# Performance work log

Hardware: AMD Instinct MI355X
Metric: run time of the kernel (lower is better)

Reference implementation:

```python
import jax, jax.numpy as jnp
import numpy as np

N_GROUP = 8
TOPK_GROUP = 4
TOP_K = 8
ROUTED_SCALE = 2.5


def setup_inputs() -> dict:
    key = jax.random.key(0)
    ks = jax.random.split(key, 8)
    B, S, D, E, I = 4, 2048, 2048, 32, 1024
    s = 0.02
    return {
        "x": jax.random.normal(ks[0], (B, S, D), jnp.float32),
        "gate_w": jax.random.normal(ks[1], (D, E), jnp.float32) * s,
        "e_bias": jnp.zeros((E,), jnp.float32),
        "gate_up": jax.random.normal(ks[2], (E, D, 2 * I), jnp.float32) * s,
        "down": jax.random.normal(ks[3], (E, I, D), jnp.float32) * s,
        "shared_gate": jax.random.normal(ks[4], (D, I), jnp.float32) * s,
        "shared_up": jax.random.normal(ks[5], (D, I), jnp.float32) * s,
        "shared_down": jax.random.normal(ks[6], (I, D), jnp.float32) * s,
    }


def _router(x_flat, gate_w, e_bias):
    N, E = x_flat.shape[0], gate_w.shape[1]
    epg = E // N_GROUP  # experts per group
    logits = x_flat @ gate_w                                   # [N, E]
    scores = jax.nn.sigmoid(logits.astype(jnp.float32))        # [N, E]
    sfr = scores + e_bias                                      # routing scores
    grouped = sfr.reshape(N, N_GROUP, epg)
    group_scores = jax.lax.top_k(grouped, min(2, epg))[0].sum(-1)   # [N, G]
    topk_group_idx = jax.lax.top_k(group_scores, TOPK_GROUP)[1]     # [N, topk_group]
    group_mask = jnp.zeros((N, N_GROUP), bool).at[
        jnp.arange(N)[:, None], topk_group_idx].set(True)
    expert_mask = jnp.repeat(group_mask, epg, axis=1)          # [N, E]
    masked = jnp.where(expert_mask, sfr, -jnp.inf)
    topk_idx = jax.lax.top_k(masked, TOP_K)[1]                 # [N, K]
    topk_w = jnp.take_along_axis(scores, topk_idx, axis=1)     # [N, K]
    topk_w = topk_w / (topk_w.sum(-1, keepdims=True) + 1e-20)  # norm_topk_prob
    topk_w = topk_w * ROUTED_SCALE
    return topk_idx, topk_w, scores


def _experts(x_flat, topk_idx, topk_w, gate_up, down):
    N, D = x_flat.shape
    E, K = gate_up.shape[0], topk_idx.shape[1]
    flat = topk_idx.reshape(-1)                                # [N*K]
    sort_idx = jnp.argsort(flat)                               # route: group rows by expert
    sorted_tokens = x_flat[sort_idx // K]                      # [N*K, D]
    group_sizes = jnp.bincount(flat, length=E).astype(jnp.int32)
    h = jax.lax.ragged_dot(sorted_tokens, gate_up, group_sizes)  # [N*K, 2I]
    gate_h, up_h = jnp.split(h, 2, axis=-1)
    inter = jax.nn.silu(gate_h) * up_h                         # SwiGLU
    out = jax.lax.ragged_dot(inter, down, group_sizes)         # [N*K, D]
    unsorted = jnp.zeros_like(out).at[sort_idx].set(out)       # unroute
    return (unsorted.reshape(N, K, D) * topk_w[..., None].astype(out.dtype)).sum(1)


def _shared_mlp(x, wg, wu, wd):
    return (jax.nn.silu(x @ wg) * (x @ wu)) @ wd


def reference(x, gate_w, e_bias, gate_up, down, shared_gate, shared_up, shared_down):
    B, S, D = x.shape
    x_flat = x.reshape(B * S, D)
    topk_idx, topk_w, scores = _router(x_flat, gate_w, e_bias)
    routed = _experts(x_flat, topk_idx, topk_w, gate_up, down).reshape(B, S, D)
    output = routed + _shared_mlp(x, shared_gate, shared_up, shared_down)
    return output, topk_idx, scores
```

## Files before the change

kernel.cpp:

```cpp
#include <hip/hip_runtime.h>
#include <hip/hip_bf16.h>
#include <math.h>


typedef __bf16 bf16_t;
typedef __bf16 bf16x8 __attribute__((ext_vector_type(8)));
typedef float  f32x4  __attribute__((ext_vector_type(4)));

constexpr int NTOK = 8192;
constexpr int D    = 2048;
constexpr int E    = 32;
constexpr int I    = 1024;
constexpr int TK   = 8;
constexpr int NK   = NTOK * TK;
constexpr int TM   = 256;
constexpr int MAX_TILES = E + NK / TM;
constexpr float RSCALE = 2.5f;

#define GL16(g, l) __builtin_amdgcn_global_load_lds( \
    (const __attribute__((address_space(1))) void*)(g), \
    (__attribute__((address_space(3))) void*)(l), 16, 0, 0)


__global__ __launch_bounds__(64) void k_zero_meta(int* counts, int* cursors, int* ntl) {
    int t = threadIdx.x;
    if (t < E) { counts[t] = 0; cursors[t] = 0; }
    if (t == 0) *ntl = 0;
}

__global__ __launch_bounds__(64) void k_sentinel(float* out) {
    if (threadIdx.x == 0) out[0] = 12345.0f;
}

__global__ __launch_bounds__(256) void k_convert_x(const float* __restrict__ src,
                                                   bf16_t* __restrict__ dst, int n8) {
    int i = blockIdx.x * 256 + threadIdx.x;
    if (i >= n8) return;
    const float4* s = (const float4*)src;
    float4 a = s[(size_t)i * 2], b = s[(size_t)i * 2 + 1];
    bf16_t t[8] = {(bf16_t)a.x, (bf16_t)a.y, (bf16_t)a.z, (bf16_t)a.w,
                   (bf16_t)b.x, (bf16_t)b.y, (bf16_t)b.z, (bf16_t)b.w};
    *(uint4*)(dst + (size_t)i * 8) = *(const uint4*)t;
}

template <int MODE>
__global__ __launch_bounds__(256) void k_transpose(const float* __restrict__ src,
                                                   bf16_t* __restrict__ dst,
                                                   int R, int C,
                                                   size_t srcMat, size_t dstMat) {
    __shared__ float t[32][33];
    int b = blockIdx.z;
    const float* s = src + (size_t)b * srcMat;
    bf16_t* d = dst + (size_t)b * dstMat;
    int c0 = blockIdx.x * 32, r0 = blockIdx.y * 32;
    int tx = threadIdx.x, ty = threadIdx.y;
#pragma unroll
    for (int yy = 0; yy < 4; yy++)
        t[ty + yy * 8][tx] = s[(size_t)(r0 + ty + yy * 8) * C + c0 + tx];
    __syncthreads();
#pragma unroll
    for (int yy = 0; yy < 4; yy++) {
        int c = c0 + ty + yy * 8;
        int rc = (MODE == 0) ? c
               : (MODE == 1) ? ((c < I) ? 2 * c : 2 * (c - I) + 1)
               : (MODE == 2) ? 2 * c : 2 * c + 1;
        d[(size_t)rc * R + r0 + tx] = (bf16_t)t[tx][ty + yy * 8];
    }
}


__global__ __launch_bounds__(256) void k_router(const float* __restrict__ x,
                                                const float* __restrict__ gw,
                                                const float* __restrict__ eb,
                                                float* __restrict__ out_idx,
                                                float* __restrict__ out_scores,
                                                float* __restrict__ topk_w,
                                                int* __restrict__ tok_expert,
                                                int* __restrict__ counts) {
    int t = blockIdx.x;
    int tid = threadIdx.x;
    int e = tid & 31, part = tid >> 5;
    const float* xr = x + (size_t)t * D;
    float partial = 0.f;
    int d0 = part * 256;
    for (int d = d0; d < d0 + 256; d++)
        partial += xr[d] * gw[(size_t)d * E + e];

    __shared__ float red[8][32];
    __shared__ float sc[32], sfr[32];
    red[part][e] = partial;
    __syncthreads();
    if (tid < 32) {
        float l = 0.f;
#pragma unroll
        for (int p = 0; p < 8; p++) l += red[p][tid];
        float s = 1.f / (1.f + expf(-l));
        sc[tid] = s;
        sfr[tid] = s + eb[tid];
        out_scores[(size_t)t * E + tid] = s;
    }
    __syncthreads();
    if (tid == 0) {
        float gs[8];
#pragma unroll
        for (int g = 0; g < 8; g++) {
            float m1 = -1e30f, m2 = -1e30f;
#pragma unroll
            for (int i = 0; i < 4; i++) {
                float v = sfr[g * 4 + i];
                if (v > m1) { m2 = m1; m1 = v; } else if (v > m2) m2 = v;
            }
            gs[g] = m1 + m2;
        }
        bool gsel[8] = {false, false, false, false, false, false, false, false};
        for (int it = 0; it < 4; it++) {
            int bi = -1; float bv = -1e30f;
            for (int g = 0; g < 8; g++)
                if (!gsel[g] && gs[g] > bv) { bv = gs[g]; bi = g; }
            gsel[bi] = true;
        }
        float masked[32];
        for (int i = 0; i < 32; i++) masked[i] = gsel[i >> 2] ? sfr[i] : -1e30f;
        int idx[TK]; float w[TK]; float wsum = 0.f;
        for (int k = 0; k < TK; k++) {
            int bi = 0; float bv = -1e30f;
            for (int i = 0; i < 32; i++)
                if (masked[i] > bv) { bv = masked[i]; bi = i; }
            masked[bi] = -1e30f;
            idx[k] = bi; w[k] = sc[bi]; wsum += w[k];
        }
        float inv = RSCALE / (wsum + 1e-20f);
        for (int k = 0; k < TK; k++) {
            out_idx[(size_t)t * TK + k] = (float)idx[k];
            topk_w[(size_t)t * TK + k] = w[k] * inv;
            tok_expert[(size_t)t * TK + k] = idx[k];
            atomicAdd(&counts[idx[k]], 1);
        }
    }
}

__global__ __launch_bounds__(64) void k_offsets(const int* __restrict__ counts,
                                                int* __restrict__ offs,
                                                int4* __restrict__ ttbl,
                                                int* __restrict__ ntl) {
    if (threadIdx.x != 0) return;
    int off = 0, nt = 0;
    for (int e = 0; e < E; e++) {
        offs[e] = off;
        int c = counts[e];
        for (int r = 0; r < c; r += TM) {
            ttbl[nt] = make_int4(off + r, min(TM, c - r), e, 0);
            nt++;
        }
        off += c;
    }
    offs[E] = off;
    *ntl = nt;
}

__global__ __launch_bounds__(256) void k_scatter(const int* __restrict__ tok_expert,
                                                 const int* __restrict__ offs,
                                                 int* __restrict__ cursors,
                                                 int* __restrict__ slot_token,
                                                 int* __restrict__ slot_inv) {
    int i = blockIdx.x * 256 + threadIdx.x;
    if (i >= NK) return;
    int e = tok_expert[i];
    int pos = offs[e] + atomicAdd(&cursors[e], 1);
    slot_token[pos] = i >> 3;
    slot_inv[i] = pos;
}


#define SCB() __builtin_amdgcn_sched_barrier(0)

#define P_MID() do { __builtin_amdgcn_s_barrier(); SCB(); \
    __builtin_amdgcn_s_setprio(1); } while (0)

#define P_END() do { __builtin_amdgcn_s_setprio(0); \
    __builtin_amdgcn_s_barrier(); SCB(); } while (0)

#define P_END_VM4() do { __builtin_amdgcn_s_setprio(0); \
    asm volatile("s_waitcnt vmcnt(4)" ::: "memory"); \
    __builtin_amdgcn_s_barrier(); SCB(); } while (0)

#define STAGE_A(b, h, k0) do { \
    GL16(gA[h][0] + (k0), smb + (b) * 65536 + (h) * 16384 + w * 1024); \
    GL16(gA[h][1] + (k0), smb + (b) * 65536 + (h) * 16384 + 8192 + w * 1024); } while (0)

#define STAGE_B(b, h, k0) do { \
    GL16(gB[h][0] + (k0), smb + (b) * 65536 + 32768 + (h) * 16384 + w * 1024); \
    GL16(gB[h][1] + (k0), smb + (b) * 65536 + 32768 + (h) * 16384 + 8192 + w * 1024); } while (0)

#define LOAD_A(b, mh) do { _Pragma("unroll") for (int m_ = 0; m_ < 4; m_++) { \
    aF[m_][0] = *(const bf16x8*)(smb + (b) * 65536 + wm * 16384 + (mh) * 8192 + m_ * 2048 + lofs0); \
    aF[m_][1] = *(const bf16x8*)(smb + (b) * 65536 + wm * 16384 + (mh) * 8192 + m_ * 2048 + lofs1); } } while (0)

#define LOAD_B(b, nh) do { _Pragma("unroll") for (int n_ = 0; n_ < 2; n_++) { \
    bF[nh][n_][0] = *(const bf16x8*)(smb + (b) * 65536 + 32768 + wn * 8192 + (nh) * 4096 + n_ * 2048 + lofs0); \
    bF[nh][n_][1] = *(const bf16x8*)(smb + (b) * 65536 + 32768 + wn * 8192 + (nh) * 4096 + n_ * 2048 + lofs1); } } while (0)

#define MM(MH, NH) do { _Pragma("unroll") for (int m_ = 0; m_ < 4; m_++) \
    _Pragma("unroll") for (int n_ = 0; n_ < 2; n_++) { \
    acc[(MH) * 4 + m_][(NH) * 2 + n_] = __builtin_amdgcn_mfma_f32_16x16x32_bf16( \
        aF[m_][0], bF[NH][n_][0], acc[(MH) * 4 + m_][(NH) * 2 + n_], 0, 0, 0); \
    acc[(MH) * 4 + m_][(NH) * 2 + n_] = __builtin_amdgcn_mfma_f32_16x16x32_bf16( \
        aF[m_][1], bF[NH][n_][1], acc[(MH) * 4 + m_][(NH) * 2 + n_], 0, 0, 0); } } while (0)

template <bool EXPERT, bool GATHER, int EPI>
__global__ __launch_bounds__(512, 2) void k_mm8(const bf16_t* __restrict__ A,
                                                const bf16_t* __restrict__ Bt,
                                                int K, size_t estride,
                                                const int* __restrict__ slot_token,
                                                const int4* __restrict__ ttbl,
                                                const int* __restrict__ ntl,
                                                void* __restrict__ C, int ldc) {
    int L = (int)blockIdx.y * 8 + (int)blockIdx.x;
    int xcd = L & 7, k = L >> 3;
    int per = (int)gridDim.y >> 3;
    int ty = xcd * per + (k >> 3);
    int tx = k & 7;

    int base_slot, rows, e;
    if (EXPERT) {
        if (ty >= *ntl) return;
        int4 tt = ttbl[ty];
        base_slot = tt.x; rows = tt.y; e = tt.z;
    } else {
        base_slot = ty * TM; rows = TM; e = 0;
    }
    int c0 = tx * 256;
    const bf16_t* Bw = Bt + (size_t)e * estride + (size_t)c0 * K;

    extern __shared__ char smb[];

    int tid = threadIdx.x, lane = tid & 63, w = tid >> 6;
    int wm = w >> 2, wn = w & 3;
    int lr = lane & 15, hi = lane >> 4;
    int rx = lr & 7;
    int lofs0 = lr * 128 + ((hi ^ rx) << 4);
    int lofs1 = lr * 128 + (((4 + hi) ^ rx) << 4);

    int srow = tid >> 3;
    int cbg = (tid & 7) ^ (srow & 7);
    const bf16_t* gA[2][2]; const bf16_t* gB[2][2];
#pragma unroll
    for (int h = 0; h < 2; h++)
#pragma unroll
        for (int rnd = 0; rnd < 2; rnd++) {
            int r = h * 128 + rnd * 64 + srow;
            int ar = min(r, rows - 1);
            int tok = GATHER ? slot_token[base_slot + ar] : (base_slot + ar);
            gA[h][rnd] = A + (size_t)tok * K + cbg * 8;
            gB[h][rnd] = Bw + (size_t)r * K + cbg * 8;
        }

    f32x4 acc[8][4] = {};
    bf16x8 aF[4][2], bF[2][2][2];

    STAGE_B(0, 0, 0); STAGE_B(0, 1, 0);
    STAGE_A(0, 0, 0); STAGE_A(0, 1, 0);
    STAGE_B(1, 0, 64); STAGE_B(1, 1, 64);
    asm volatile("s_waitcnt vmcnt(4)" ::: "memory");
    __builtin_amdgcn_s_barrier();
    SCB();

    int nt = K >> 6;
    for (int kt = 0; kt < nt; kt += 2) {
        int k1 = (kt + 1) << 6;
        int k2 = (kt + 2 < nt) ? (kt + 2) << 6 : 0;
        int k3 = (kt + 3 < nt) ? (kt + 3) << 6 : 0;
        LOAD_B(0, 0); LOAD_A(0, 0);
        STAGE_A(1, 0, k1);
        P_MID(); MM(0, 0); P_END();
        LOAD_B(0, 1);
        STAGE_A(1, 1, k1);
        P_MID(); MM(0, 1); P_END();
        LOAD_A(0, 1);
        STAGE_B(0, 0, k2);
        P_MID(); MM(1, 0); P_END();
        STAGE_B(0, 1, k2);
        P_MID(); MM(1, 1); P_END_VM4();
        LOAD_B(1, 0); LOAD_A(1, 0);
        STAGE_A(0, 0, k2);
        P_MID(); MM(0, 0); P_END();
        LOAD_B(1, 1);
        STAGE_A(0, 1, k2);
        P_MID(); MM(0, 1); P_END();
        LOAD_A(1, 1);
        STAGE_B(1, 0, k3);
        P_MID(); MM(1, 0); P_END();
        STAGE_B(1, 1, k3);
        P_MID(); MM(1, 1); P_END_VM4();
    }

#pragma unroll
    for (int mi = 0; mi < 8; mi++) {
#pragma unroll
        for (int j = 0; j < 4; j++) {
            int r = wm * 128 + mi * 16 + hi * 4 + j;
            bool valid = !EXPERT || (r < rows);
            size_t orow = (size_t)base_slot + r;
#pragma unroll
            for (int f = 0; f < 4; f++) {
                float v = acc[mi][f][j];
                int c = c0 + wn * 64 + f * 16 + lr;
                if (EPI == 0) {
                    float o = __shfl_xor(v, 1);
                    float g = (lane & 1) ? o : v;
                    float u = (lane & 1) ? v : o;
                    float sv = g / (1.f + __expf(-g)) * u;
                    if (valid && !(lane & 1))
                        ((bf16_t*)C)[orow * ldc + (c >> 1)] = (bf16_t)sv;
                } else if (EPI == 1) {
                    float o = __shfl_xor(v, 1);
                    if (valid && !(lane & 1)) {
                        bf16_t pr[2] = {(bf16_t)v, (bf16_t)o};
                        *(unsigned int*)((bf16_t*)C + orow * ldc + c) = *(unsigned int*)pr;
                    }
                } else {
                    if (valid) ((float*)C)[orow * ldc + c] = v;
                }
            }
        }
    }
}


__global__ __launch_bounds__(256) void k_finalize(const bf16_t* __restrict__ outS,
                                                  const int* __restrict__ slot_inv,
                                                  const float* __restrict__ tkw,
                                                  float* __restrict__ out) {
    int tok = blockIdx.x, tid = threadIdx.x;
    __shared__ int sp[TK];
    __shared__ float swt[TK];
    if (tid < TK) {
        sp[tid] = slot_inv[tok * TK + tid];
        swt[tid] = tkw[tok * TK + tid];
    }
    __syncthreads();
    int c = tid * 8;
    float* op = out + (size_t)tok * D + c;
    float acc[8];
    float4 o0 = *(float4*)op, o1 = *(float4*)(op + 4);
    acc[0] = o0.x; acc[1] = o0.y; acc[2] = o0.z; acc[3] = o0.w;
    acc[4] = o1.x; acc[5] = o1.y; acc[6] = o1.z; acc[7] = o1.w;
#pragma unroll
    for (int k = 0; k < TK; k++) {
        bf16x8 v = *(const bf16x8*)(outS + (size_t)sp[k] * D + c);
        float w = swt[k];
#pragma unroll
        for (int j = 0; j < 8; j++) acc[j] += w * (float)v[j];
    }
    o0 = make_float4(acc[0], acc[1], acc[2], acc[3]);
    o1 = make_float4(acc[4], acc[5], acc[6], acc[7]);
    *(float4*)op = o0;
    *(float4*)(op + 4) = o1;
}


extern "C" void kernel_launch(void* const* d_in, const int* in_sizes, int n_in,
                              void* d_out, int out_size, void* d_ws, size_t ws_size,
                              hipStream_t stream) {
    const float* x  = (const float*)d_in[0];
    const float* gw = (const float*)d_in[1];
    const float* eb = (const float*)d_in[2];
    const float* gu = (const float*)d_in[3];
    const float* dn = (const float*)d_in[4];
    const float* sg = (const float*)d_in[5];
    const float* su = (const float*)d_in[6];
    const float* sd = (const float*)d_in[7];

    float* out        = (float*)d_out;
    float* out_idx    = out + (size_t)NTOK * D;
    float* out_scores = out_idx + (size_t)NTOK * TK;

    char* w = (char*)d_ws;
    auto alloc = [&](size_t bytes) {
        char* p = w;
        w += (bytes + 255) & ~(size_t)255;
        return p;
    };
    bf16_t* xb      = (bf16_t*)alloc((size_t)NTOK * D * 2);
    bf16_t* gut     = (bf16_t*)alloc((size_t)E * 2 * I * D * 2);
    bf16_t* dnt     = (bf16_t*)alloc((size_t)E * D * I * 2);
    bf16_t* sh1t    = (bf16_t*)alloc((size_t)2 * I * D * 2);
    bf16_t* sdt     = (bf16_t*)alloc((size_t)D * I * 2);
    bf16_t* inter   = (bf16_t*)alloc((size_t)NK * I * 2);
    bf16_t* inter_s = (bf16_t*)alloc((size_t)NTOK * I * 2);
    float*  tkw     = (float*)alloc((size_t)NK * 4);
    int*    tke     = (int*)alloc((size_t)NK * 4);
    int*    stok    = (int*)alloc((size_t)NK * 4);
    int*    sinv    = (int*)alloc((size_t)NK * 4);
    int*    counts  = (int*)alloc(E * 4);
    int*    offs    = (int*)alloc((E + 1) * 4);
    int*    curs    = (int*)alloc(E * 4);
    int4*   ttbl    = (int4*)alloc(MAX_TILES * 16);
    int*    ntl     = (int*)alloc(4);
    bf16_t* outS    = gut;

    if ((size_t)(w - (char*)d_ws) > ws_size) {
        k_sentinel<<<1, 64, 0, stream>>>(out);
        return;
    }

    k_zero_meta<<<1, 64, 0, stream>>>(counts, curs, ntl);
    k_convert_x<<<(NTOK * D / 8 + 255) / 256, 256, 0, stream>>>(x, xb, NTOK * D / 8);

    k_transpose<1><<<dim3(2 * I / 32, D / 32, E), dim3(32, 8), 0, stream>>>(
        gu, gut, D, 2 * I, (size_t)D * 2 * I, (size_t)D * 2 * I);
    k_transpose<0><<<dim3(D / 32, I / 32, E), dim3(32, 8), 0, stream>>>(
        dn, dnt, I, D, (size_t)I * D, (size_t)I * D);
    k_transpose<2><<<dim3(I / 32, D / 32, 1), dim3(32, 8), 0, stream>>>(
        sg, sh1t, D, I, 0, 0);
    k_transpose<3><<<dim3(I / 32, D / 32, 1), dim3(32, 8), 0, stream>>>(
        su, sh1t, D, I, 0, 0);
    k_transpose<0><<<dim3(D / 32, I / 32, 1), dim3(32, 8), 0, stream>>>(
        sd, sdt, I, D, 0, 0);

    k_router<<<NTOK, 256, 0, stream>>>(x, gw, eb, out_idx, out_scores, tkw, tke, counts);
    k_offsets<<<1, 64, 0, stream>>>(counts, offs, ttbl, ntl);
    k_scatter<<<NK / 256, 256, 0, stream>>>(tke, offs, curs, stok, sinv);

    constexpr size_t SMEM = 131072;
    k_mm8<true, true, 0><<<dim3(8, MAX_TILES), 512, SMEM, stream>>>(
        xb, gut, D, (size_t)2 * I * D, stok, ttbl, ntl, inter, I);
    k_mm8<true, false, 1><<<dim3(8, MAX_TILES), 512, SMEM, stream>>>(
        inter, dnt, I, (size_t)D * I, stok, ttbl, ntl, outS, D);

    k_mm8<false, false, 0><<<dim3(8, NTOK / TM), 512, SMEM, stream>>>(
        xb, sh1t, D, 0, nullptr, nullptr, nullptr, inter_s, I);
    k_mm8<false, false, 2><<<dim3(8, NTOK / TM), 512, SMEM, stream>>>(
        inter_s, sdt, I, 0, nullptr, nullptr, nullptr, out, D);

    k_finalize<<<NTOK, 256, 0, stream>>>(outS, sinv, tkw, out);
}
```

Before: 1.857 ms.

## Restructure GEMM main loop with one barrier per phase and double-buffered B fragments

Rewrites the inner k-loop schedule of the grouped GEMM kernel so each phase has a single barrier, preceded by a vmcnt(4) wait, instead of two barriers. B register fragments are now double-buffered (b0/b1) so LDS reads for the next MFMA block overlap the current one. A-tile staging is reordered by row-round rather than by half. The loop also prefetches the first fragments before entering. The aim is to cut barrier stalls and hide LDS latency behind MFMAs. This adds register pressure and risks LDS race hazards if the buffer reuse ordering is wrong.

```diff
diff --git a/kernel.cpp b/kernel.cpp
--- a/kernel.cpp
+++ b/kernel.cpp
@@ -174,38 +174,34 @@
 
 #define SCB() __builtin_amdgcn_sched_barrier(0)
 
-#define P_MID() do { __builtin_amdgcn_s_barrier(); SCB(); \
-    __builtin_amdgcn_s_setprio(1); } while (0)
-
-#define P_END() do { __builtin_amdgcn_s_setprio(0); \
+#define PEND() do { asm volatile("s_waitcnt vmcnt(4)" ::: "memory"); \
     __builtin_amdgcn_s_barrier(); SCB(); } while (0)
 
-#define P_END_VM4() do { __builtin_amdgcn_s_setprio(0); \
-    asm volatile("s_waitcnt vmcnt(4)" ::: "memory"); \
-    __builtin_amdgcn_s_barrier(); SCB(); } while (0)
-
-#define STAGE_A(b, h, k0) do { \
-    GL16(gA[h][0] + (k0), smb + (b) * 65536 + (h) * 16384 + w * 1024); \
-    GL16(gA[h][1] + (k0), smb + (b) * 65536 + (h) * 16384 + 8192 + w * 1024); } while (0)
-
-#define STAGE_B(b, h, k0) do { \
+#define SA2(b, rnd, k0) do { \
+    GL16(gA[0][rnd] + (k0), smb + (b) * 65536 + (rnd) * 8192 + w * 1024); \
+    GL16(gA[1][rnd] + (k0), smb + (b) * 65536 + 16384 + (rnd) * 8192 + w * 1024); } while (0)
+
+#define SB(b, h, k0) do { \
     GL16(gB[h][0] + (k0), smb + (b) * 65536 + 32768 + (h) * 16384 + w * 1024); \
     GL16(gB[h][1] + (k0), smb + (b) * 65536 + 32768 + (h) * 16384 + 8192 + w * 1024); } while (0)
 
-#define LOAD_A(b, mh) do { _Pragma("unroll") for (int m_ = 0; m_ < 4; m_++) { \
+#define LDA(b, mh) do { _Pragma("unroll") for (int m_ = 0; m_ < 4; m_++) { \
     aF[m_][0] = *(const bf16x8*)(smb + (b) * 65536 + wm * 16384 + (mh) * 8192 + m_ * 2048 + lofs0); \
     aF[m_][1] = *(const bf16x8*)(smb + (b) * 65536 + wm * 16384 + (mh) * 8192 + m_ * 2048 + lofs1); } } while (0)
 
-#define LOAD_B(b, nh) do { _Pragma("unroll") for (int n_ = 0; n_ < 2; n_++) { \
-    bF[nh][n_][0] = *(const bf16x8*)(smb + (b) * 65536 + 32768 + wn * 8192 + (nh) * 4096 + n_ * 2048 + lofs0); \
-    bF[nh][n_][1] = *(const bf16x8*)(smb + (b) * 65536 + 32768 + wn * 8192 + (nh) * 4096 + n_ * 2048 + lofs1); } } while (0)
-
-#define MM(MH, NH) do { _Pragma("unroll") for (int m_ = 0; m_ < 4; m_++) \
+#define LDB(dst, b, nh) do { _Pragma("unroll") for (int n_ = 0; n_ < 2; n_++) { \
+    dst[n_][0] = *(const bf16x8*)(smb + (b) * 65536 + 32768 + wn * 8192 + (nh) * 4096 + n_ * 2048 + lofs0); \
+    dst[n_][1] = *(const bf16x8*)(smb + (b) * 65536 + 32768 + wn * 8192 + (nh) * 4096 + n_ * 2048 + lofs1); } } while (0)
+
+#define MMA(bv, MH, NH) do { \
+    __builtin_amdgcn_s_setprio(1); \
+    _Pragma("unroll") for (int m_ = 0; m_ < 4; m_++) \
     _Pragma("unroll") for (int n_ = 0; n_ < 2; n_++) { \
     acc[(MH) * 4 + m_][(NH) * 2 + n_] = __builtin_amdgcn_mfma_f32_16x16x32_bf16( \
-        aF[m_][0], bF[NH][n_][0], acc[(MH) * 4 + m_][(NH) * 2 + n_], 0, 0, 0); \
+        aF[m_][0], bv[n_][0], acc[(MH) * 4 + m_][(NH) * 2 + n_], 0, 0, 0); \
     acc[(MH) * 4 + m_][(NH) * 2 + n_] = __builtin_amdgcn_mfma_f32_16x16x32_bf16( \
-        aF[m_][1], bF[NH][n_][1], acc[(MH) * 4 + m_][(NH) * 2 + n_], 0, 0, 0); } } while (0)
+        aF[m_][1], bv[n_][1], acc[(MH) * 4 + m_][(NH) * 2 + n_], 0, 0, 0); } \
+    __builtin_amdgcn_s_setprio(0); } while (0)
 
 template <bool EXPERT, bool GATHER, int EPI>
 __global__ __launch_bounds__(512, 2) void k_mm8(const bf16_t* __restrict__ A,
@@ -256,42 +252,52 @@
         }
 
     f32x4 acc[8][4] = {};
-    bf16x8 aF[4][2], bF[2][2][2];
-
-    STAGE_B(0, 0, 0); STAGE_B(0, 1, 0);
-    STAGE_A(0, 0, 0); STAGE_A(0, 1, 0);
-    STAGE_B(1, 0, 64); STAGE_B(1, 1, 64);
-    asm volatile("s_waitcnt vmcnt(4)" ::: "memory");
+    bf16x8 aF[4][2], b0[2][2], b1[2][2];
+
+    SA2(0, 0, 0); SA2(0, 1, 0);
+    SB(0, 0, 0); SB(0, 1, 0);
+    SA2(1, 0, 64);
+    SB(1, 0, 64); SB(1, 1, 64);
+    asm volatile("s_waitcnt vmcnt(0)" ::: "memory");
     __builtin_amdgcn_s_barrier();
     SCB();
+    LDA(0, 0); LDB(b0, 0, 0);
 
     int nt = K >> 6;
     for (int kt = 0; kt < nt; kt += 2) {
         int k1 = (kt + 1) << 6;
         int k2 = (kt + 2 < nt) ? (kt + 2) << 6 : 0;
         int k3 = (kt + 3 < nt) ? (kt + 3) << 6 : 0;
-        LOAD_B(0, 0); LOAD_A(0, 0);
-        STAGE_A(1, 0, k1);
-        P_MID(); MM(0, 0); P_END();
-        LOAD_B(0, 1);
-        STAGE_A(1, 1, k1);
-        P_MID(); MM(0, 1); P_END();
-        LOAD_A(0, 1);
-        STAGE_B(0, 0, k2);
-        P_MID(); MM(1, 0); P_END();
-        STAGE_B(0, 1, k2);
-        P_MID(); MM(1, 1); P_END_VM4();
-        LOAD_B(1, 0); LOAD_A(1, 0);
-        STAGE_A(0, 0, k2);
-        P_MID(); MM(0, 0); P_END();
-        LOAD_B(1, 1);
-        STAGE_A(0, 1, k2);
-        P_MID(); MM(0, 1); P_END();
-        LOAD_A(1, 1);
-        STAGE_B(1, 0, k3);
-        P_MID(); MM(1, 0); P_END();
-        STAGE_B(1, 1, k3);
-        P_MID(); MM(1, 1); P_END_VM4();
+        LDB(b1, 0, 1);
+        MMA(b0, 0, 0);
+        SA2(1, 1, k1);
+        PEND();
+        MMA(b1, 0, 1);
+        LDA(0, 1);
+        SA2(0, 0, k2);
+        PEND();
+        MMA(b0, 1, 0);
+        SB(0, 0, k2);
+        PEND();
+        MMA(b1, 1, 1);
+        LDA(1, 0); LDB(b0, 1, 0);
+        SB(0, 1, k2);
+        PEND();
+        LDB(b1, 1, 1);
+        MMA(b0, 0, 0);
+        SA2(0, 1, k2);
+        PEND();
+        MMA(b1, 0, 1);
+        LDA(1, 1);
+        SA2(1, 0, k3);
+        PEND();
+        MMA(b0, 1, 0);
+        SB(1, 0, k3);
+        PEND();
+        MMA(b1, 1, 1);
+        LDA(0, 0); LDB(b0, 0, 0);
+        SB(1, 1, k3);
+        PEND();
     }
 
 #pragma unroll
```

New measurement: 1.821 ms (median of 4 runs). -2.0%, faster.
